# Performance work log

Hardware: AMD Instinct MI355X
Metric: run time of the kernel (lower is better)

Reference implementation:

```python
import jax, jax.numpy as jnp
import numpy as np

B, N, D, H = 4, 2048, 1024, 16
HD = D // H
LR_SCALE = 0.01  # base step size for the fast-weight test-time update
EPS = 1e-6


def setup_inputs() -> dict:
    key = jax.random.key(0)
    ks = jax.random.split(key, 11)
    s = 0.02
    x = jax.random.normal(ks[0], (B, N, D), jnp.float32)
    Wq = jax.random.normal(ks[1], (D, D), jnp.float32) * s
    Wk = jax.random.normal(ks[2], (D, D), jnp.float32) * s
    Wv = jax.random.normal(ks[3], (D, D), jnp.float32) * s
    Wo = jax.random.normal(ks[4], (D, D), jnp.float32) * s
    w1_init = jax.random.normal(ks[5], (H, HD, HD), jnp.float32) * s  # FastWeightGLU init state
    w3_init = jax.random.normal(ks[6], (H, HD, HD), jnp.float32) * s
    W_lr = jax.random.normal(ks[7], (D, H), jnp.float32) * s  # FastWeightHpGLU lr head
    norm_w = jnp.ones((D,), jnp.float32)  # grouped RMSNorm weight
    Wg1 = jax.random.normal(ks[8], (D, HD), jnp.float32) * s  # output_gate bottleneck
    Wg2 = jax.random.normal(ks[9], (HD, D), jnp.float32) * s
    return dict(x=x, Wq=Wq, Wk=Wk, Wv=Wv, Wo=Wo, w1_init=w1_init,
                w3_init=w3_init, W_lr=W_lr, norm_w=norm_w, Wg1=Wg1, Wg2=Wg2)


def _fast_weight_train(q, k, v, lr, w1_init, w3_init):
    # q,k,v: (b,n,h,hd); lr: (b,n,h); fast weight f(x) = silu(x@W1) * (x@W3)
    b = q.shape[0]
    W1_0 = jnp.broadcast_to(w1_init, (b,) + w1_init.shape)
    W3_0 = jnp.broadcast_to(w3_init, (b,) + w3_init.shape)

    def step(carry, inp):
        W1, W3 = carry
        q_t, k_t, v_t, lr_t = inp  # (b,h,hd), lr_t: (b,h,1)
        h1 = jnp.einsum('bhd,bhde->bhe', k_t, W1)
        h3 = jnp.einsum('bhd,bhde->bhe', k_t, W3)
        sg = jax.nn.sigmoid(h1)
        s1 = h1 * sg  # silu(h1)
        err = s1 * h3 - v_t  # d(0.5||f(k)-v||^2)/df
        dsilu = sg * (1.0 + h1 * (1.0 - sg))
        g1 = err * h3 * dsilu
        g3 = err * s1
        W1 = W1 - lr_t[..., None] * jnp.einsum('bhd,bhe->bhde', k_t, g1)
        W3 = W3 - lr_t[..., None] * jnp.einsum('bhd,bhe->bhde', k_t, g3)
        o1 = jnp.einsum('bhd,bhde->bhe', q_t, W1)
        o3 = jnp.einsum('bhd,bhde->bhe', q_t, W3)
        return (W1, W3), jax.nn.silu(o1) * o3

    xs = (q.transpose(1, 0, 2, 3), k.transpose(1, 0, 2, 3),
          v.transpose(1, 0, 2, 3), lr.transpose(1, 0, 2)[..., None])
    (W1, W3), outs = jax.lax.scan(step, (W1_0, W3_0), xs)
    return outs.transpose(1, 0, 2, 3), (W1, W3)  # (b,n,h,hd)


def reference(x, Wq, Wk, Wv, Wo, w1_init, w3_init, W_lr, norm_w, Wg1, Wg2):
    b, n, d = x.shape
    h = w1_init.shape[0]
    hd = d // h
    q = jax.nn.silu((x @ Wq).reshape(b, n, h, hd))
    k = jax.nn.silu((x @ Wk).reshape(b, n, h, hd))
    v = (x @ Wv).reshape(b, n, h, hd)
    lr = LR_SCALE * jax.nn.sigmoid(x @ W_lr)  # (b,n,h) per-token hyper-param
    out, _ = _fast_weight_train(q, k, v, lr, w1_init, w3_init)
    # grouped RMSNorm (per head) fused with sigmoid output gate
    rms = jax.lax.rsqrt(jnp.mean(out * out, axis=-1, keepdims=True) + EPS)
    out = (out * rms).reshape(b, n, d) * norm_w
    gate = (x @ Wg1) @ Wg2
    out = out * jax.nn.sigmoid(gate)
    return out @ Wo
```

## Files before the change

### kernel.cpp

```cpp
#include <hip/hip_runtime.h>
#include <hip/hip_bf16.h>

#define B_ 4
#define N_ 2048
#define D_ 1024
#define H_ 16
#define HD_ 64
#define MTOT (B_*N_)
#define CH_ 16
#define NCH_ (N_/CH_)

typedef __attribute__((ext_vector_type(8))) short short8v;
typedef __attribute__((ext_vector_type(4))) float f32x4;

__device__ __forceinline__ float fsig(float x){
  return __builtin_amdgcn_rcpf(1.0f + __expf(-x));
}

__global__ void k_cast_bf16(const float* __restrict__ in, __hip_bfloat16* __restrict__ out, int n4){
  int i = blockIdx.x*256 + threadIdx.x;
  if (i >= n4) return;
  float4 vv = ((const float4*)in)[i];
  __hip_bfloat16 b0 = __float2bfloat16(vv.x), b1 = __float2bfloat16(vv.y),
                 b2 = __float2bfloat16(vv.z), b3 = __float2bfloat16(vv.w);
  ushort4 o;
  o.x = *(const unsigned short*)&b0; o.y = *(const unsigned short*)&b1;
  o.z = *(const unsigned short*)&b2; o.w = *(const unsigned short*)&b3;
  ((ushort4*)out)[i] = o;
}

__global__ void k_transpose_cast(const float* __restrict__ in, __hip_bfloat16* __restrict__ out,
                                 int R, int C){
  __shared__ float tile[64][65];
  int r0 = blockIdx.y*64, c0 = blockIdx.x*64;
  int tid = threadIdx.x;
  #pragma unroll
  for (int i=0;i<16;i++){ int idx = tid + i*256; int rr = idx>>6, cc = idx&63;
    tile[rr][cc] = in[(size_t)(r0+rr)*C + (c0+cc)]; }
  __syncthreads();
  #pragma unroll
  for (int i=0;i<16;i++){ int idx = tid + i*256; int rr = idx>>6, cc = idx&63;
    out[(size_t)(c0+rr)*R + (r0+cc)] = __float2bfloat16(tile[cc][rr]); }
}

__global__ void k_prep_wgl(const float* __restrict__ Wg1, const float* __restrict__ Wlr,
                           __hip_bfloat16* __restrict__ WgL){
  int idx = blockIdx.x*256 + threadIdx.x;
  int r = idx >> 10, d = idx & 1023;
  float v = 0.f;
  if (r < 64) v = Wg1[(size_t)d*64 + r];
  else if (r < 80) v = Wlr[(size_t)d*16 + (r-64)];
  WgL[idx] = __float2bfloat16(v);
}

__global__ void k_post_gl(const float* __restrict__ proj, __hip_bfloat16* __restrict__ t1,
                          float* __restrict__ lrout){
  int m = blockIdx.x*4 + (threadIdx.x>>6);
  int e = threadIdx.x & 63;
  float val = proj[(size_t)m*128 + e];
  t1[(size_t)m*64 + e] = __float2bfloat16(val);
  if (e < 16){
    float s = proj[(size_t)m*128 + 64 + e];
    lrout[(size_t)m*16 + e] = 0.01f*fsig(s);
  }
}

__device__ __forceinline__ void gl2lds16(const void* g, void* l){
  __builtin_amdgcn_global_load_lds((const __attribute__((address_space(1))) void*)g,
                                   (__attribute__((address_space(3))) void*)l, 16, 0, 0);
}

template<int ACT, int LAYOUT>
__global__ __launch_bounds__(256,2) void k_gemm_bt2(
    const __hip_bfloat16* __restrict__ A, const __hip_bfloat16* __restrict__ BT,
    float* __restrict__ C, int M, int N, int K)
{
  __shared__ short As[128*32];
  __shared__ short Bs[128*32];
  const int n0 = blockIdx.x*128, m0 = blockIdx.y*128;
  const int tid = threadIdx.x, lane = tid & 63, wid = tid >> 6;
  const int wm = wid >> 1, wn = wid & 1;
  const short* Aps = (const short*)A;
  const short* Bps = (const short*)BT;
  f32x4 acc[4][4] = {};
  const int srow = wid*32 + (lane>>2);
  const int scol = (lane&3)*8;
  const size_t aoff0 = (size_t)(m0+srow)*K + scol;
  const size_t boff0 = (size_t)(n0+srow)*K + scol;
  short* lA = As + wid*1024;
  short* lB = Bs + wid*1024;
  const int row = lane & 15, kq = (lane >> 4)*8;
  for (int kk = 0; kk < K; kk += 32) {
    __syncthreads();
    gl2lds16(Aps + aoff0 + kk,                 lA);
    gl2lds16(Aps + aoff0 + (size_t)16*K + kk,  lA + 512);
    gl2lds16(Bps + boff0 + kk,                 lB);
    gl2lds16(Bps + boff0 + (size_t)16*K + kk,  lB + 512);
    __syncthreads();
    short8v af[4], bfr[4];
    #pragma unroll
    for (int i=0;i<4;i++) af[i]  = *(const short8v*)(As + (wm*64 + i*16 + row)*32 + kq);
    #pragma unroll
    for (int j=0;j<4;j++) bfr[j] = *(const short8v*)(Bs + (wn*64 + j*16 + row)*32 + kq);
    #pragma unroll
    for (int i=0;i<4;i++)
      #pragma unroll
      for (int j=0;j<4;j++)
        acc[i][j] = __builtin_amdgcn_mfma_f32_16x16x32_bf16(af[i], bfr[j], acc[i][j], 0, 0, 0);
  }
  #pragma unroll
  for (int i=0;i<4;i++){
    #pragma unroll
    for (int j=0;j<4;j++){
      int col = n0 + wn*64 + j*16 + (lane & 15);
      #pragma unroll
      for (int qq=0; qq<4; ++qq){
        int rowg = m0 + wm*64 + i*16 + (lane>>4)*4 + qq;
        float val = acc[i][j][qq];
        if (LAYOUT==0) {
          if (ACT==1) val = val*fsig(val);
          C[(size_t)rowg*N + col] = val;
        } else {
          const int t3 = col >> 10, cc2 = col & 1023;
          if (t3 < 2) val = val*fsig(val);
          size_t oidx = (size_t)t3*((size_t)MTOT*D_)
                      + ((((size_t)(rowg>>11))*16 + (cc2>>6))*(size_t)N_ + (size_t)(rowg & 2047))*64
                      + (size_t)(cc2 & 63);
          ((__hip_bfloat16*)C)[oidx] = __float2bfloat16(val);
        }
      }
    }
  }
}

__device__ __forceinline__ unsigned short bfr16(float x){
  __hip_bfloat16 b = __float2bfloat16(x);
  return *(unsigned short*)&b;
}

__global__ __launch_bounds__(256,1) void k_scan13(
    const __hip_bfloat16* __restrict__ q, const __hip_bfloat16* __restrict__ k,
    const __hip_bfloat16* __restrict__ v, const float* __restrict__ lr,
    const float* __restrict__ w1i, const float* __restrict__ w3i,
    float* __restrict__ so)
{
  const int blk = blockIdx.x;
  const int bh  = blk >> 2;
  const int sl  = blk & 3;
  const int b = bh >> 4, h = bh & 15;
  const int e0 = sl*16;
  const int tid = threadIdx.x, lane = tid & 63, wid = tid >> 6;
  const int tA = lane & 15, ks8 = (lane >> 4)*8;

  __shared__ __align__(16) __hip_bfloat16 Wb1[16*64];
  __shared__ __align__(16) __hip_bfloat16 Wb3[16*64];
  __shared__ __align__(16) float KW1e[256], KW3e[256];
  __shared__ __align__(16) float QW1[2][256], QW3[2][256];
  __shared__ __align__(16) float GKK[256];
  __shared__ __align__(16) float GQK[2][256];
  __shared__ __align__(16) float C13[2][512];
  __shared__ __align__(16) float kS[16][68];

  const int we = tid & 15;
  const int wd = (tid >> 4) * 4;
  float w1r[4], w3r[4];
  {
    const float* w1p = w1i + (size_t)h*HD_*HD_ + e0 + we;
    const float* w3p = w3i + (size_t)h*HD_*HD_ + e0 + we;
    #pragma unroll
    for (int j=0;j<4;j++){ w1r[j] = w1p[(size_t)(wd+j)*64]; w3r[j] = w3p[(size_t)(wd+j)*64]; }
  }
  const int mir_off = we*128 + ((wd*2) ^ ((we&7)<<4));
  auto write_mirrors = [&](){
    uint2 p1, p3;
    p1.x = (unsigned)bfr16(w1r[0]) | ((unsigned)bfr16(w1r[1])<<16);
    p1.y = (unsigned)bfr16(w1r[2]) | ((unsigned)bfr16(w1r[3])<<16);
    p3.x = (unsigned)bfr16(w3r[0]) | ((unsigned)bfr16(w3r[1])<<16);
    p3.y = (unsigned)bfr16(w3r[2]) | ((unsigned)bfr16(w3r[3])<<16);
    *(uint2*)((char*)Wb1 + mir_off) = p1;
    *(uint2*)((char*)Wb3 + mir_off) = p3;
  };
  write_mirrors();

  const short* kps = (const short*)(k + (size_t)bh*N_*64);
  const short* qps = (const short*)(q + (size_t)bh*N_*64);
  const __hip_bfloat16* vfb = v + (size_t)bh*N_*64;
  const float* lrp = lr + ((size_t)b*N_)*16 + h;
  float* sob = so + (((size_t)b*N_)*16 + h)*64 + e0;

  auto mir_read = [&](const __hip_bfloat16* Wm, int m)->short8v{
    return *(const short8v*)((const char*)Wm + tA*128 + (((m*32+ks8)*2) ^ ((tA&7)<<4)));
  };

  short8v pK0, pK1;
  short8v pQ0, pQ1;
  float  vvr[16], lrr[16];

  if (wid==1 || wid==3){
    pK0 = *(const short8v*)(kps + (size_t)tA*64 + ks8);
    pK1 = *(const short8v*)(kps + (size_t)tA*64 + 32 + ks8);
  }
  if (wid==2 || wid==3){
    pQ0 = *(const short8v*)(qps + (size_t)tA*64 + ks8);
    pQ1 = *(const short8v*)(qps + (size_t)tA*64 + 32 + ks8);
  }
  if (wid==0 && lane < 16) {
    #pragma unroll
    for (int t=0;t<CH_;++t){
      vvr[t] = __bfloat162float(vfb[(size_t)t*64 + e0 + lane]);
      lrr[t] = lrp[(size_t)t*16];
    }
  }
  __syncthreads();

  #pragma unroll 1
  for (int c = 0; c < NCH_; ++c) {
    const int t0 = c*CH_;
    const int par = c & 1;

    if (wid == 1) {
      float kf_[16];
      #pragma unroll
      for (int j=0;j<4;j++){
        unsigned u = ((const unsigned*)&pK0)[j];
        kf_[2*j]   = __uint_as_float(u << 16);
        kf_[2*j+1] = __uint_as_float(u & 0xffff0000u);
      }
      #pragma unroll
      for (int j=0;j<4;j++){
        unsigned u = ((const unsigned*)&pK1)[j];
        kf_[8+2*j]   = __uint_as_float(u << 16);
        kf_[8+2*j+1] = __uint_as_float(u & 0xffff0000u);
      }
      f32x4 s0 = {kf_[0],kf_[1],kf_[2],kf_[3]};   *(f32x4*)&kS[tA][ks8]      = s0;
      f32x4 s1 = {kf_[4],kf_[5],kf_[6],kf_[7]};   *(f32x4*)&kS[tA][ks8+4]    = s1;
      f32x4 s2 = {kf_[8],kf_[9],kf_[10],kf_[11]}; *(f32x4*)&kS[tA][32+ks8]   = s2;
      f32x4 s3 = {kf_[12],kf_[13],kf_[14],kf_[15]};*(f32x4*)&kS[tA][32+ks8+4]= s3;
      const int slot = (((lane>>4)*4) ^ (((tA>>1)&3)<<2));
      f32x4 acc = {};
      acc = __builtin_amdgcn_mfma_f32_16x16x32_bf16(pK0, mir_read(Wb1,0), acc, 0,0,0);
      acc = __builtin_amdgcn_mfma_f32_16x16x32_bf16(pK1, mir_read(Wb1,1), acc, 0,0,0);
      *(f32x4*)&KW1e[tA*16 + slot] = acc;
      f32x4 ac3 = {};
      ac3 = __builtin_amdgcn_mfma_f32_16x16x32_bf16(pK0, mir_read(Wb3,0), ac3, 0,0,0);
      ac3 = __builtin_amdgcn_mfma_f32_16x16x32_bf16(pK1, mir_read(Wb3,1), ac3, 0,0,0);
      *(f32x4*)&KW3e[tA*16 + slot] = ac3;
    } else if (wid == 2) {
      f32x4 acc = {};
      acc = __builtin_amdgcn_mfma_f32_16x16x32_bf16(pQ0, mir_read(Wb1,0), acc, 0,0,0);
      acc = __builtin_amdgcn_mfma_f32_16x16x32_bf16(pQ1, mir_read(Wb1,1), acc, 0,0,0);
      #pragma unroll
      for (int qq=0;qq<4;++qq) QW1[par][((lane>>4)*4+qq)*16 + tA] = acc[qq];
      f32x4 ac3 = {};
      ac3 = __builtin_amdgcn_mfma_f32_16x16x32_bf16(pQ0, mir_read(Wb3,0), ac3, 0,0,0);
      ac3 = __builtin_amdgcn_mfma_f32_16x16x32_bf16(pQ1, mir_read(Wb3,1), ac3, 0,0,0);
      #pragma unroll
      for (int qq=0;qq<4;++qq) QW3[par][((lane>>4)*4+qq)*16 + tA] = ac3[qq];
    } else if (wid == 3) {
      f32x4 acc = {};
      acc = __builtin_amdgcn_mfma_f32_16x16x32_bf16(pK0, pK0, acc, 0,0,0);
      acc = __builtin_amdgcn_mfma_f32_16x16x32_bf16(pK1, pK1, acc, 0,0,0);
      #pragma unroll
      for (int qq=0;qq<4;++qq) GKK[((lane>>4)*4+qq)*16 + tA] = acc[qq];
      f32x4 ac2 = {};
      ac2 = __builtin_amdgcn_mfma_f32_16x16x32_bf16(pQ0, pK0, ac2, 0,0,0);
      ac2 = __builtin_amdgcn_mfma_f32_16x16x32_bf16(pQ1, pK1, ac2, 0,0,0);
      #pragma unroll
      for (int qq=0;qq<4;++qq) GQK[par][((lane>>4)*4+qq)*16 + tA] = ac2[qq];
    }
    __syncthreads();

    const int tn0 = ((c+1 < NCH_) ? c+1 : c) * CH_;
    if (wid >= 1) {
      if (wid==1 || wid==3){
        pK0 = *(const short8v*)(kps + (size_t)(tn0+tA)*64 + ks8);
        pK1 = *(const short8v*)(kps + (size_t)(tn0+tA)*64 + 32 + ks8);
      }
      if (wid==2 || wid==3){
        pQ0 = *(const short8v*)(qps + (size_t)(tn0+tA)*64 + ks8);
        pQ1 = *(const short8v*)(qps + (size_t)(tn0+tA)*64 + 32 + ks8);
      }
      if (c > 0) {
        const int parp = par ^ 1;
        const int bt = t0 - CH_;
        const int p0 = tid - 64;
        #pragma unroll
        for (int rep=0; rep<2; ++rep){
          const int pp = p0 + rep*192;
          if (pp < 256){
            const int ot = pp >> 4, oe = pp & 15;
            float o1 = QW1[parp][ot*16+oe], o3 = QW3[parp][ot*16+oe];
            #pragma unroll
            for (int s = 0; s < CH_; ++s) {
              const float gl2 = GQK[parp][ot*16+s];
              const float2 cc = *(const float2*)&C13[parp][(s*16+oe)*2];
              const float g = (s <= ot) ? gl2 : 0.0f;
              o1 = fmaf(-g, cc.x, o1);
              o3 = fmaf(-g, cc.y, o3);
            }
            sob[(size_t)(bt+ot)*(H_*HD_) + oe] = (o1*fsig(o1))*o3;
          }
        }
      }
    } else if (lane < 16) {
      float vvn[16], lrn[16];
      #pragma unroll
      for (int t=0;t<CH_;++t){
        vvn[t] = __bfloat162float(vfb[(size_t)(tn0+t)*64 + e0 + lane]);
        lrn[t] = lrp[(size_t)(tn0+t)*16];
      }
      float a1[16], a3[16];
      const int swr = ((lane>>1)&3)<<2;
      #pragma unroll
      for (int i2=0;i2<4;i2++){
        f32x4 x1 = *(const f32x4*)&KW1e[lane*16 + ((i2*4) ^ swr)];
        f32x4 x3 = *(const f32x4*)&KW3e[lane*16 + ((i2*4) ^ swr)];
        a1[i2*4+0]=x1[0]; a1[i2*4+1]=x1[1]; a1[i2*4+2]=x1[2]; a1[i2*4+3]=x1[3];
        a3[i2*4+0]=x3[0]; a3[i2*4+1]=x3[1]; a3[i2*4+2]=x3[2]; a3[i2*4+3]=x3[3];
      }
      f32x4 grow[3][4];
      #pragma unroll
      for (int i2=0;i2<4;i2++){
        grow[0][i2] = *(const f32x4*)&GKK[ 0 + i2*4];
        grow[1][i2] = *(const f32x4*)&GKK[16 + i2*4];
        grow[2][i2] = *(const f32x4*)&GKK[32 + i2*4];
      }
      #pragma unroll
      for (int t = 0; t < CH_; ++t) {
        const float h1 = a1[t], h3 = a3[t];
        const float sg = fsig(h1);
        const float s1 = h1*sg;
        const float er = fmaf(s1, h3, -vvr[t]);
        const float ds = sg*fmaf(h1, 1.0f - sg, 1.0f);
        const float lt = lrr[t];
        float2 cc; cc.x = lt*(er*h3*ds); cc.y = lt*(er*s1);
        *(float2*)&C13[par][(t*16+lane)*2] = cc;
        #pragma unroll
        for (int t2 = t+1; t2 < CH_; ++t2) {
          const float g = grow[t%3][t2>>2][t2&3];
          a1[t2] = fmaf(-g, cc.x, a1[t2]);
          a3[t2] = fmaf(-g, cc.y, a3[t2]);
        }
        if (t + 3 < CH_) {
          #pragma unroll
          for (int i2=0;i2<4;i2++) grow[(t+3)%3][i2] = *(const f32x4*)&GKK[(t+3)*16 + i2*4];
        }
      }
      #pragma unroll
      for (int t=0;t<CH_;++t){ vvr[t]=vvn[t]; lrr[t]=lrn[t]; }
    }
    __syncthreads();

    #pragma unroll
    for (int s = 0; s < CH_; ++s) {
      const float2 cc = *(const float2*)&C13[par][(s*16+we)*2];
      const float4 ks = *(const float4*)&kS[s][wd];
      w1r[0] = fmaf(-ks.x, cc.x, w1r[0]); w1r[1] = fmaf(-ks.y, cc.x, w1r[1]);
      w1r[2] = fmaf(-ks.z, cc.x, w1r[2]); w1r[3] = fmaf(-ks.w, cc.x, w1r[3]);
      w3r[0] = fmaf(-ks.x, cc.y, w3r[0]); w3r[1] = fmaf(-ks.y, cc.y, w3r[1]);
      w3r[2] = fmaf(-ks.z, cc.y, w3r[2]); w3r[3] = fmaf(-ks.w, cc.y, w3r[3]);
    }
    write_mirrors();
    __syncthreads();
  }

  if (wid >= 1) {
    const int parp = (NCH_-1) & 1;
    const int bt = (NCH_-1)*CH_;
    const int p0 = tid - 64;
    #pragma unroll
    for (int rep=0; rep<2; ++rep){
      const int pp = p0 + rep*192;
      if (pp < 256){
        const int ot = pp >> 4, oe = pp & 15;
        float o1 = QW1[parp][ot*16+oe], o3 = QW3[parp][ot*16+oe];
        #pragma unroll
        for (int s = 0; s < CH_; ++s) {
          const float gl2 = GQK[parp][ot*16+s];
          const float2 cc = *(const float2*)&C13[parp][(s*16+oe)*2];
          const float g = (s <= ot) ? gl2 : 0.0f;
          o1 = fmaf(-g, cc.x, o1);
          o3 = fmaf(-g, cc.y, o3);
        }
        sob[(size_t)(bt+ot)*(H_*HD_) + oe] = (o1*fsig(o1))*o3;
      }
    }
  }
}

__global__ void k_norm_gate(const float* __restrict__ so, const float* __restrict__ gate,
                            const float* __restrict__ nw, __hip_bfloat16* __restrict__ y)
{
  int idx = blockIdx.x*4 + (threadIdx.x>>6);
  int e = threadIdx.x & 63;
  float o = so[(size_t)idx*64 + e];
  float ss = o*o;
  #pragma unroll
  for (int m=32; m>=1; m>>=1) ss += __shfl_xor(ss, m, 64);
  float rms = rsqrtf(ss*(1.0f/64.0f) + 1e-6f);
  int hh = idx & 15;
  size_t bn = (size_t)(idx >> 4);
  int d = hh*64 + e;
  float g = gate[bn*1024 + d];
  float val = o*rms*nw[d] * fsig(g);
  y[bn*1024 + d] = __float2bfloat16(val);
}

extern "C" void kernel_launch(void* const* d_in, const int* in_sizes, int n_in,
                              void* d_out, int out_size, void* d_ws, size_t ws_size,
                              hipStream_t stream)
{
  const float* x   = (const float*)d_in[0];
  const float* Wq  = (const float*)d_in[1];
  const float* Wk  = (const float*)d_in[2];
  const float* Wv  = (const float*)d_in[3];
  const float* Wo  = (const float*)d_in[4];
  const float* w1i = (const float*)d_in[5];
  const float* w3i = (const float*)d_in[6];
  const float* Wlr = (const float*)d_in[7];
  const float* nw  = (const float*)d_in[8];
  const float* Wg1 = (const float*)d_in[9];
  const float* Wg2 = (const float*)d_in[10];
  float* out = (float*)d_out;

  char* p = (char*)d_ws;
  auto take = [&](size_t bytes)->void*{ void* r = (void*)p; p += (bytes + 255) & ~(size_t)255; return r; };
  __hip_bfloat16* xb    = (__hip_bfloat16*)take((size_t)MTOT*D_*2);
  __hip_bfloat16* WqkvT = (__hip_bfloat16*)take((size_t)3*D_*D_*2);
  __hip_bfloat16* Wot   = (__hip_bfloat16*)take((size_t)D_*D_*2);
  __hip_bfloat16* Wg2t  = (__hip_bfloat16*)take((size_t)D_*HD_*2);
  __hip_bfloat16* WgL   = (__hip_bfloat16*)take((size_t)128*D_*2);
  __hip_bfloat16* t1b   = (__hip_bfloat16*)take((size_t)MTOT*HD_*2);
  float* projt = (float*)take((size_t)MTOT*128*4);
  __hip_bfloat16* qb = (__hip_bfloat16*)take((size_t)MTOT*D_*2);
  __hip_bfloat16* kb = (__hip_bfloat16*)take((size_t)MTOT*D_*2);
  __hip_bfloat16* vb = (__hip_bfloat16*)take((size_t)MTOT*D_*2);
  float* lrb = (float*)take((size_t)MTOT*H_*4);
  float* sob = (float*)take((size_t)MTOT*D_*4);
  __hip_bfloat16* yb = (__hip_bfloat16*)take((size_t)MTOT*D_*2);

  k_cast_bf16<<<MTOT*D_/4/256, 256, 0, stream>>>(x, xb, MTOT*D_/4);
  k_transpose_cast<<<dim3(16,16), 256, 0, stream>>>(Wq, WqkvT,             D_, D_);
  k_transpose_cast<<<dim3(16,16), 256, 0, stream>>>(Wk, WqkvT + D_*D_,     D_, D_);
  k_transpose_cast<<<dim3(16,16), 256, 0, stream>>>(Wv, WqkvT + 2*D_*D_,   D_, D_);
  k_transpose_cast<<<dim3(16,16), 256, 0, stream>>>(Wo, Wot, D_, D_);
  k_transpose_cast<<<dim3(16,1),  256, 0, stream>>>(Wg2, Wg2t, HD_, D_);
  k_prep_wgl<<<512, 256, 0, stream>>>(Wg1, Wlr, WgL);
  k_gemm_bt2<0,0><<<dim3(1,64), 256, 0, stream>>>(xb, WgL, projt, MTOT, 128, D_);
  k_post_gl<<<MTOT/4, 256, 0, stream>>>(projt, t1b, lrb);
  k_gemm_bt2<1,2><<<dim3(24,64), 256, 0, stream>>>(xb, WqkvT, (float*)qb, MTOT, 3*D_, D_);
  k_gemm_bt2<0,0><<<dim3(8,64), 256, 0, stream>>>(t1b, Wg2t, out, MTOT, D_, HD_);
  k_scan13<<<256, 256, 0, stream>>>(qb, kb, vb, lrb, w1i, w3i, sob);
  k_norm_gate<<<MTOT*H_/4, 256, 0, stream>>>(sob, out, nw, yb);
  k_gemm_bt2<0,0><<<dim3(8,64), 256, 0, stream>>>(yb, Wot, out, MTOT, D_, D_);
}
```

Baseline: 497.7 us.

## Keep fast-weight state in MFMA fragment registers and pipeline scan phases

The per-head fast weights W1/W3 now live directly in the registers of waves 1 and 2, laid out as MFMA B-operand fragments, instead of being mirrored to LDS as bf16 and re-read each chunk. The weight update, fragment rebuild and next chunk's MFMA projections (KW, QW, Gram matrices) are moved to the end of the iteration with double-buffered kS. This removes one of three block barriers per chunk; the other two become a custom lgkmcnt-wait barrier. Work is spread so wave 1 owns W1 and wave 2 owns W3, at the cost of more register pressure and redundant per-wave K/Q loads.

```diff
diff --git a/kernel.cpp b/kernel.cpp
--- a/kernel.cpp
+++ b/kernel.cpp
@@ -15,6 +15,12 @@
 
 __device__ __forceinline__ float fsig(float x){
   return __builtin_amdgcn_rcpf(1.0f + __expf(-x));
+}
+
+__device__ __forceinline__ void bar_lgkm(){
+  asm volatile("s_waitcnt lgkmcnt(0)" ::: "memory");
+  __builtin_amdgcn_sched_barrier(0);
+  __builtin_amdgcn_s_barrier();
 }
 
 __global__ void k_cast_bf16(const float* __restrict__ in, __hip_bfloat16* __restrict__ out, int n4){
@@ -138,7 +144,7 @@
   return *(unsigned short*)&b;
 }
 
-__global__ __launch_bounds__(256,1) void k_scan13(
+__global__ __launch_bounds__(256,1) void k_scan14(
     const __hip_bfloat16* __restrict__ q, const __hip_bfloat16* __restrict__ k,
     const __hip_bfloat16* __restrict__ v, const float* __restrict__ lr,
     const float* __restrict__ w1i, const float* __restrict__ w3i,
@@ -150,37 +156,14 @@
   const int b = bh >> 4, h = bh & 15;
   const int e0 = sl*16;
   const int tid = threadIdx.x, lane = tid & 63, wid = tid >> 6;
-  const int tA = lane & 15, ks8 = (lane >> 4)*8;
-
-  __shared__ __align__(16) __hip_bfloat16 Wb1[16*64];
-  __shared__ __align__(16) __hip_bfloat16 Wb3[16*64];
+  const int tA = lane & 15, g = lane >> 4;
+  const int ks8 = g*8;
+
   __shared__ __align__(16) float KW1e[256], KW3e[256];
   __shared__ __align__(16) float QW1[2][256], QW3[2][256];
-  __shared__ __align__(16) float GKK[256];
-  __shared__ __align__(16) float GQK[2][256];
+  __shared__ __align__(16) float GKK[256], GQK[2][256];
   __shared__ __align__(16) float C13[2][512];
-  __shared__ __align__(16) float kS[16][68];
-
-  const int we = tid & 15;
-  const int wd = (tid >> 4) * 4;
-  float w1r[4], w3r[4];
-  {
-    const float* w1p = w1i + (size_t)h*HD_*HD_ + e0 + we;
-    const float* w3p = w3i + (size_t)h*HD_*HD_ + e0 + we;
-    #pragma unroll
-    for (int j=0;j<4;j++){ w1r[j] = w1p[(size_t)(wd+j)*64]; w3r[j] = w3p[(size_t)(wd+j)*64]; }
-  }
-  const int mir_off = we*128 + ((wd*2) ^ ((we&7)<<4));
-  auto write_mirrors = [&](){
-    uint2 p1, p3;
-    p1.x = (unsigned)bfr16(w1r[0]) | ((unsigned)bfr16(w1r[1])<<16);
-    p1.y = (unsigned)bfr16(w1r[2]) | ((unsigned)bfr16(w1r[3])<<16);
-    p3.x = (unsigned)bfr16(w3r[0]) | ((unsigned)bfr16(w3r[1])<<16);
-    p3.y = (unsigned)bfr16(w3r[2]) | ((unsigned)bfr16(w3r[3])<<16);
-    *(uint2*)((char*)Wb1 + mir_off) = p1;
-    *(uint2*)((char*)Wb3 + mir_off) = p3;
-  };
-  write_mirrors();
+  __shared__ __align__(16) float kS[2][16][68];
 
   const short* kps = (const short*)(k + (size_t)bh*N_*64);
   const short* qps = (const short*)(q + (size_t)bh*N_*64);
@@ -188,100 +171,105 @@
   const float* lrp = lr + ((size_t)b*N_)*16 + h;
   float* sob = so + (((size_t)b*N_)*16 + h)*64 + e0;
 
-  auto mir_read = [&](const __hip_bfloat16* Wm, int m)->short8v{
-    return *(const short8v*)((const char*)Wm + tA*128 + (((m*32+ks8)*2) ^ ((tA&7)<<4)));
+  float wm[2][8];
+  short8v wf0, wf1;
+  short8v pK0,pK1,pQ0,pQ1;
+  short8v nK0,nK1,nQ0,nQ1;
+  float vvr[16], lrr[16];
+
+  float* KWe = (wid==2) ? KW3e : KW1e;
+
+  auto rebuild_frags = [&](){
+    short8v r0, r1;
+    #pragma unroll
+    for (int j=0;j<8;j++){ r0[j]=(short)bfr16(wm[0][j]); r1[j]=(short)bfr16(wm[1][j]); }
+    wf0 = r0; wf1 = r1;
   };
 
-  short8v pK0, pK1;
-  short8v pQ0, pQ1;
-  float  vvr[16], lrr[16];
-
-  if (wid==1 || wid==3){
+  auto store_kS = [&](int buf, short8v K0, short8v K1){
+    float kf_[16];
+    #pragma unroll
+    for (int j2=0;j2<4;j2++){
+      unsigned u = ((const unsigned*)&K0)[j2];
+      kf_[2*j2]   = __uint_as_float(u << 16);
+      kf_[2*j2+1] = __uint_as_float(u & 0xffff0000u);
+    }
+    #pragma unroll
+    for (int j2=0;j2<4;j2++){
+      unsigned u = ((const unsigned*)&K1)[j2];
+      kf_[8+2*j2]   = __uint_as_float(u << 16);
+      kf_[8+2*j2+1] = __uint_as_float(u & 0xffff0000u);
+    }
+    f32x4 s0 = {kf_[0],kf_[1],kf_[2],kf_[3]};    *(f32x4*)&kS[buf][tA][ks8]      = s0;
+    f32x4 s1 = {kf_[4],kf_[5],kf_[6],kf_[7]};    *(f32x4*)&kS[buf][tA][ks8+4]    = s1;
+    f32x4 s2 = {kf_[8],kf_[9],kf_[10],kf_[11]};  *(f32x4*)&kS[buf][tA][32+ks8]   = s2;
+    f32x4 s3 = {kf_[12],kf_[13],kf_[14],kf_[15]};*(f32x4*)&kS[buf][tA][32+ks8+4] = s3;
+  };
+
+  auto do_A = [&](int pbuf, short8v K0, short8v K1, short8v Q0, short8v Q1){
+    if (wid==1 || wid==2){
+      const int slot = (g*4) ^ (((tA>>1)&3)<<2);
+      f32x4 acc = {};
+      acc = __builtin_amdgcn_mfma_f32_16x16x32_bf16(K0, wf0, acc, 0,0,0);
+      acc = __builtin_amdgcn_mfma_f32_16x16x32_bf16(K1, wf1, acc, 0,0,0);
+      *(f32x4*)&KWe[tA*16 + slot] = acc;
+      f32x4 ac2 = {};
+      ac2 = __builtin_amdgcn_mfma_f32_16x16x32_bf16(Q0, wf0, ac2, 0,0,0);
+      ac2 = __builtin_amdgcn_mfma_f32_16x16x32_bf16(Q1, wf1, ac2, 0,0,0);
+      float* QW = (wid==1) ? QW1[pbuf] : QW3[pbuf];
+      #pragma unroll
+      for (int qq=0;qq<4;++qq) QW[(g*4+qq)*16 + tA] = ac2[qq];
+    } else if (wid==3){
+      f32x4 acc = {};
+      acc = __builtin_amdgcn_mfma_f32_16x16x32_bf16(K0, K0, acc, 0,0,0);
+      acc = __builtin_amdgcn_mfma_f32_16x16x32_bf16(K1, K1, acc, 0,0,0);
+      #pragma unroll
+      for (int qq=0;qq<4;++qq) GKK[(g*4+qq)*16 + tA] = acc[qq];
+      f32x4 ac2 = {};
+      ac2 = __builtin_amdgcn_mfma_f32_16x16x32_bf16(Q0, K0, ac2, 0,0,0);
+      ac2 = __builtin_amdgcn_mfma_f32_16x16x32_bf16(Q1, K1, ac2, 0,0,0);
+      #pragma unroll
+      for (int qq=0;qq<4;++qq) GQK[pbuf][(g*4+qq)*16 + tA] = ac2[qq];
+    }
+  };
+
+  if (wid==1 || wid==2){
+    const float* wp = ((wid==1)? w1i : w3i) + (size_t)h*HD_*HD_ + e0 + tA;
+    #pragma unroll
+    for (int m=0;m<2;m++)
+      #pragma unroll
+      for (int j=0;j<8;j++)
+        wm[m][j] = wp[(size_t)(m*32 + g*8 + j)*64];
+    rebuild_frags();
+  }
+  if (wid>=1){
     pK0 = *(const short8v*)(kps + (size_t)tA*64 + ks8);
     pK1 = *(const short8v*)(kps + (size_t)tA*64 + 32 + ks8);
-  }
-  if (wid==2 || wid==3){
     pQ0 = *(const short8v*)(qps + (size_t)tA*64 + ks8);
     pQ1 = *(const short8v*)(qps + (size_t)tA*64 + 32 + ks8);
-  }
-  if (wid==0 && lane < 16) {
+  } else if (lane < 16){
     #pragma unroll
     for (int t=0;t<CH_;++t){
       vvr[t] = __bfloat162float(vfb[(size_t)t*64 + e0 + lane]);
       lrr[t] = lrp[(size_t)t*16];
     }
   }
-  __syncthreads();
+  if (wid==1) store_kS(0, pK0, pK1);
+  if (wid>=1) do_A(0, pK0, pK1, pQ0, pQ1);
 
   #pragma unroll 1
   for (int c = 0; c < NCH_; ++c) {
     const int t0 = c*CH_;
-    const int par = c & 1;
-
-    if (wid == 1) {
-      float kf_[16];
-      #pragma unroll
-      for (int j=0;j<4;j++){
-        unsigned u = ((const unsigned*)&pK0)[j];
-        kf_[2*j]   = __uint_as_float(u << 16);
-        kf_[2*j+1] = __uint_as_float(u & 0xffff0000u);
-      }
-      #pragma unroll
-      for (int j=0;j<4;j++){
-        unsigned u = ((const unsigned*)&pK1)[j];
-        kf_[8+2*j]   = __uint_as_float(u << 16);
-        kf_[8+2*j+1] = __uint_as_float(u & 0xffff0000u);
-      }
-      f32x4 s0 = {kf_[0],kf_[1],kf_[2],kf_[3]};   *(f32x4*)&kS[tA][ks8]      = s0;
-      f32x4 s1 = {kf_[4],kf_[5],kf_[6],kf_[7]};   *(f32x4*)&kS[tA][ks8+4]    = s1;
-      f32x4 s2 = {kf_[8],kf_[9],kf_[10],kf_[11]}; *(f32x4*)&kS[tA][32+ks8]   = s2;
-      f32x4 s3 = {kf_[12],kf_[13],kf_[14],kf_[15]};*(f32x4*)&kS[tA][32+ks8+4]= s3;
-      const int slot = (((lane>>4)*4) ^ (((tA>>1)&3)<<2));
-      f32x4 acc = {};
-      acc = __builtin_amdgcn_mfma_f32_16x16x32_bf16(pK0, mir_read(Wb1,0), acc, 0,0,0);
-      acc = __builtin_amdgcn_mfma_f32_16x16x32_bf16(pK1, mir_read(Wb1,1), acc, 0,0,0);
-      *(f32x4*)&KW1e[tA*16 + slot] = acc;
-      f32x4 ac3 = {};
-      ac3 = __builtin_amdgcn_mfma_f32_16x16x32_bf16(pK0, mir_read(Wb3,0), ac3, 0,0,0);
-      ac3 = __builtin_amdgcn_mfma_f32_16x16x32_bf16(pK1, mir_read(Wb3,1), ac3, 0,0,0);
-      *(f32x4*)&KW3e[tA*16 + slot] = ac3;
-    } else if (wid == 2) {
-      f32x4 acc = {};
-      acc = __builtin_amdgcn_mfma_f32_16x16x32_bf16(pQ0, mir_read(Wb1,0), acc, 0,0,0);
-      acc = __builtin_amdgcn_mfma_f32_16x16x32_bf16(pQ1, mir_read(Wb1,1), acc, 0,0,0);
-      #pragma unroll
-      for (int qq=0;qq<4;++qq) QW1[par][((lane>>4)*4+qq)*16 + tA] = acc[qq];
-      f32x4 ac3 = {};
-      ac3 = __builtin_amdgcn_mfma_f32_16x16x32_bf16(pQ0, mir_read(Wb3,0), ac3, 0,0,0);
-      ac3 = __builtin_amdgcn_mfma_f32_16x16x32_bf16(pQ1, mir_read(Wb3,1), ac3, 0,0,0);
-      #pragma unroll
-      for (int qq=0;qq<4;++qq) QW3[par][((lane>>4)*4+qq)*16 + tA] = ac3[qq];
-    } else if (wid == 3) {
-      f32x4 acc = {};
-      acc = __builtin_amdgcn_mfma_f32_16x16x32_bf16(pK0, pK0, acc, 0,0,0);
-      acc = __builtin_amdgcn_mfma_f32_16x16x32_bf16(pK1, pK1, acc, 0,0,0);
-      #pragma unroll
-      for (int qq=0;qq<4;++qq) GKK[((lane>>4)*4+qq)*16 + tA] = acc[qq];
-      f32x4 ac2 = {};
-      ac2 = __builtin_amdgcn_mfma_f32_16x16x32_bf16(pQ0, pK0, ac2, 0,0,0);
-      ac2 = __builtin_amdgcn_mfma_f32_16x16x32_bf16(pQ1, pK1, ac2, 0,0,0);
-      #pragma unroll
-      for (int qq=0;qq<4;++qq) GQK[par][((lane>>4)*4+qq)*16 + tA] = ac2[qq];
-    }
-    __syncthreads();
+    const int par = c & 1, parn = par ^ 1;
+    bar_lgkm();
 
     const int tn0 = ((c+1 < NCH_) ? c+1 : c) * CH_;
     if (wid >= 1) {
-      if (wid==1 || wid==3){
-        pK0 = *(const short8v*)(kps + (size_t)(tn0+tA)*64 + ks8);
-        pK1 = *(const short8v*)(kps + (size_t)(tn0+tA)*64 + 32 + ks8);
-      }
-      if (wid==2 || wid==3){
-        pQ0 = *(const short8v*)(qps + (size_t)(tn0+tA)*64 + ks8);
-        pQ1 = *(const short8v*)(qps + (size_t)(tn0+tA)*64 + 32 + ks8);
-      }
+      nK0 = *(const short8v*)(kps + (size_t)(tn0+tA)*64 + ks8);
+      nK1 = *(const short8v*)(kps + (size_t)(tn0+tA)*64 + 32 + ks8);
+      nQ0 = *(const short8v*)(qps + (size_t)(tn0+tA)*64 + ks8);
+      nQ1 = *(const short8v*)(qps + (size_t)(tn0+tA)*64 + 32 + ks8);
       if (c > 0) {
-        const int parp = par ^ 1;
         const int bt = t0 - CH_;
         const int p0 = tid - 64;
         #pragma unroll
@@ -289,14 +277,14 @@
           const int pp = p0 + rep*192;
           if (pp < 256){
             const int ot = pp >> 4, oe = pp & 15;
-            float o1 = QW1[parp][ot*16+oe], o3 = QW3[parp][ot*16+oe];
+            float o1 = QW1[parn][ot*16+oe], o3 = QW3[parn][ot*16+oe];
             #pragma unroll
             for (int s = 0; s < CH_; ++s) {
-              const float gl2 = GQK[parp][ot*16+s];
-              const float2 cc = *(const float2*)&C13[parp][(s*16+oe)*2];
-              const float g = (s <= ot) ? gl2 : 0.0f;
-              o1 = fmaf(-g, cc.x, o1);
-              o3 = fmaf(-g, cc.y, o3);
+              const float gl2 = GQK[parn][ot*16+s];
+              const float2 cc = *(const float2*)&C13[parn][(s*16+oe)*2];
+              const float gm = (s <= ot) ? gl2 : 0.0f;
+              o1 = fmaf(-gm, cc.x, o1);
+              o3 = fmaf(-gm, cc.y, o3);
             }
             sob[(size_t)(bt+ot)*(H_*HD_) + oe] = (o1*fsig(o1))*o3;
           }
@@ -337,9 +325,9 @@
         *(float2*)&C13[par][(t*16+lane)*2] = cc;
         #pragma unroll
         for (int t2 = t+1; t2 < CH_; ++t2) {
-          const float g = grow[t%3][t2>>2][t2&3];
-          a1[t2] = fmaf(-g, cc.x, a1[t2]);
-          a3[t2] = fmaf(-g, cc.y, a3[t2]);
+          const float gm = grow[t%3][t2>>2][t2&3];
+          a1[t2] = fmaf(-gm, cc.x, a1[t2]);
+          a3[t2] = fmaf(-gm, cc.y, a3[t2]);
         }
         if (t + 3 < CH_) {
           #pragma unroll
@@ -349,19 +337,34 @@
       #pragma unroll
       for (int t=0;t<CH_;++t){ vvr[t]=vvn[t]; lrr[t]=lrn[t]; }
     }
-    __syncthreads();
-
-    #pragma unroll
-    for (int s = 0; s < CH_; ++s) {
-      const float2 cc = *(const float2*)&C13[par][(s*16+we)*2];
-      const float4 ks = *(const float4*)&kS[s][wd];
-      w1r[0] = fmaf(-ks.x, cc.x, w1r[0]); w1r[1] = fmaf(-ks.y, cc.x, w1r[1]);
-      w1r[2] = fmaf(-ks.z, cc.x, w1r[2]); w1r[3] = fmaf(-ks.w, cc.x, w1r[3]);
-      w3r[0] = fmaf(-ks.x, cc.y, w3r[0]); w3r[1] = fmaf(-ks.y, cc.y, w3r[1]);
-      w3r[2] = fmaf(-ks.z, cc.y, w3r[2]); w3r[3] = fmaf(-ks.w, cc.y, w3r[3]);
-    }
-    write_mirrors();
-    __syncthreads();
+    bar_lgkm();
+
+    if (c+1 < NCH_) {
+      if (wid==1 || wid==2){
+        const int off = (wid==2) ? 1 : 0;
+        #pragma unroll
+        for (int s=0;s<CH_;++s){
+          const float cs = C13[par][(s*16+tA)*2 + off];
+          const f32x4 ka = *(const f32x4*)&kS[par][s][ks8];
+          const f32x4 kb = *(const f32x4*)&kS[par][s][ks8+4];
+          const f32x4 kc = *(const f32x4*)&kS[par][s][32+ks8];
+          const f32x4 kd = *(const f32x4*)&kS[par][s][32+ks8+4];
+          wm[0][0]=fmaf(-ka[0],cs,wm[0][0]); wm[0][1]=fmaf(-ka[1],cs,wm[0][1]);
+          wm[0][2]=fmaf(-ka[2],cs,wm[0][2]); wm[0][3]=fmaf(-ka[3],cs,wm[0][3]);
+          wm[0][4]=fmaf(-kb[0],cs,wm[0][4]); wm[0][5]=fmaf(-kb[1],cs,wm[0][5]);
+          wm[0][6]=fmaf(-kb[2],cs,wm[0][6]); wm[0][7]=fmaf(-kb[3],cs,wm[0][7]);
+          wm[1][0]=fmaf(-kc[0],cs,wm[1][0]); wm[1][1]=fmaf(-kc[1],cs,wm[1][1]);
+          wm[1][2]=fmaf(-kc[2],cs,wm[1][2]); wm[1][3]=fmaf(-kc[3],cs,wm[1][3]);
+          wm[1][4]=fmaf(-kd[0],cs,wm[1][4]); wm[1][5]=fmaf(-kd[1],cs,wm[1][5]);
+          wm[1][6]=fmaf(-kd[2],cs,wm[1][6]); wm[1][7]=fmaf(-kd[3],cs,wm[1][7]);
+        }
+        rebuild_frags();
+        if (wid==1) store_kS(parn, nK0, nK1);
+        do_A(parn, nK0, nK1, nQ0, nQ1);
+      } else if (wid==3){
+        do_A(parn, nK0, nK1, nQ0, nQ1);
+      }
+    }
   }
 
   if (wid >= 1) {
@@ -378,9 +381,9 @@
         for (int s = 0; s < CH_; ++s) {
           const float gl2 = GQK[parp][ot*16+s];
           const float2 cc = *(const float2*)&C13[parp][(s*16+oe)*2];
-          const float g = (s <= ot) ? gl2 : 0.0f;
-          o1 = fmaf(-g, cc.x, o1);
-          o3 = fmaf(-g, cc.y, o3);
+          const float gm = (s <= ot) ? gl2 : 0.0f;
+          o1 = fmaf(-gm, cc.x, o1);
+          o3 = fmaf(-gm, cc.y, o3);
         }
         sob[(size_t)(bt+ot)*(H_*HD_) + oe] = (o1*fsig(o1))*o3;
       }
@@ -450,7 +453,7 @@
   k_post_gl<<<MTOT/4, 256, 0, stream>>>(projt, t1b, lrb);
   k_gemm_bt2<1,2><<<dim3(24,64), 256, 0, stream>>>(xb, WqkvT, (float*)qb, MTOT, 3*D_, D_);
   k_gemm_bt2<0,0><<<dim3(8,64), 256, 0, stream>>>(t1b, Wg2t, out, MTOT, D_, HD_);
-  k_scan13<<<256, 256, 0, stream>>>(qb, kb, vb, lrb, w1i, w3i, sob);
+  k_scan14<<<256, 256, 0, stream>>>(qb, kb, vb, lrb, w1i, w3i, sob);
   k_norm_gate<<<MTOT*H_/4, 256, 0, stream>>>(sob, out, nw, yb);
   k_gemm_bt2<0,0><<<dim3(8,64), 256, 0, stream>>>(yb, Wot, out, MTOT, D_, D_);
 }
```

After: 616.6 us. +23.9%, slower.
